# Performance work log

Hardware: AMD Instinct MI355X
Metric: run time of the kernel (lower is better)

The kernel has to match this reference:

```python
import jax, jax.numpy as jnp
import numpy as np

H = 2048        # hidden_size
NH = 32         # num_attention_heads
HD = H // NH    # head_dim
I = 8192        # intermediate_size
L = 2           # num_hidden_layers
B, S = 1, 2048
EPS = 1e-5


def _layernorm(x, gamma):
    # keras LayerNormalization(center=False): mean-subtract, var-normalize, scale by gamma (no beta)
    mu = jnp.mean(x, axis=-1, keepdims=True)
    var = jnp.mean(jnp.square(x - mu), axis=-1, keepdims=True)
    return (x - mu) * jax.lax.rsqrt(var + EPS) * gamma


def _gelu_tanh(x):
    return 0.5 * x * (1.0 + jnp.tanh(0.7978845608028654 * x * (1.0 + 0.044715 * x * x)))


def setup_inputs() -> dict:
    key = jax.random.key(0)
    ks = jax.random.split(key, 12)
    sd = 0.02
    inputs_embeds = jax.random.normal(ks[0], (B, S, H), dtype=jnp.float32)
    attention_mask = jnp.tril(jnp.ones((S, S), dtype=bool))[None, None]  # causal [1,1,S,S]
    return {
        "inputs_embeds": inputs_embeds,
        "attention_mask": attention_mask,
        "Wq": jax.random.normal(ks[1], (L, H, H), jnp.float32) * sd,
        "Wk": jax.random.normal(ks[2], (L, H, H), jnp.float32) * sd,
        "Wv": jax.random.normal(ks[3], (L, H, H), jnp.float32) * sd,
        "Wo": jax.random.normal(ks[4], (L, H, H), jnp.float32) * sd,
        "bo": jnp.zeros((L, H), jnp.float32),
        "W1": jax.random.normal(ks[5], (L, H, I), jnp.float32) * sd,
        "W2": jax.random.normal(ks[6], (L, I, H), jnp.float32) * sd,
        "b2": jnp.zeros((L, H), jnp.float32),
        "g1": jnp.ones((L, H), jnp.float32),
        "g2": jnp.ones((L, H), jnp.float32),
        "gf": jnp.ones((H,), jnp.float32),
    }


def _forward(inputs_embeds, attention_mask, Wq, Wk, Wv, Wo, bo, W1, W2, b2, g1, g2, gf):
    x = inputs_embeds
    scale = 1.0 / jnp.sqrt(jnp.float32(HD))
    for l in range(L):
        # --- attention block ---
        h = _layernorm(x, g1[l])
        q = h @ Wq[l]
        k = h @ Wk[l]
        v = h @ Wv[l]
        # split heads: [B,S,H] -> [B,NH,S,HD]
        q = q.reshape(B, S, NH, HD).transpose(0, 2, 1, 3)
        k = k.reshape(B, S, NH, HD).transpose(0, 2, 1, 3)
        v = v.reshape(B, S, NH, HD).transpose(0, 2, 1, 3)
        scores = jnp.einsum("bhqd,bhkd->bhqk", q, k) * scale
        scores = jnp.where(attention_mask, scores, jnp.float32(-1e9))
        probs = jax.nn.softmax(scores, axis=-1)
        ctx = jnp.einsum("bhqk,bhkd->bhqd", probs, v)
        ctx = ctx.transpose(0, 2, 1, 3).reshape(B, S, H)
        x = x + (ctx @ Wo[l] + bo[l])
        # --- MLP block ---
        h = _layernorm(x, g2[l])
        h = _gelu_tanh(h @ W1[l]) @ W2[l] + b2[l]
        x = x + h
    return _layernorm(x, gf)


def reference(inputs_embeds, attention_mask, Wq, Wk, Wv, Wo, bo, W1, W2, b2, g1, g2, gf):
    return _forward(inputs_embeds, attention_mask, Wq, Wk, Wv, Wo, bo, W1, W2, b2, g1, g2, gf)
```

## Files before the change

### kernel.cpp

```cpp
#include <hip/hip_runtime.h>
#include <hip/hip_bf16.h>
#include <stdint.h>


#define H_   2048
#define NH_  32
#define HD_  64
#define I_   8192
#define L_   2
#define S_   2048
#define EPS_ 1e-5f

typedef _Float16 f16;
typedef __attribute__((ext_vector_type(8))) _Float16 f16x8;
typedef __attribute__((ext_vector_type(4))) float   f32x4;

#define BF16_PROBE 0x3F803F80u

static __device__ __forceinline__ float bf2f(unsigned short b) {
  return __uint_as_float(((unsigned int)b) << 16);
}

static __device__ __forceinline__ float gelu_f(float x) {
  float y = 0.7978845608028654f * x * (1.0f + 0.044715f * x * x);
  return x / (1.0f + __expf(-2.0f * y));
}

#define GLDS(gp, lp)                                                          \
  __builtin_amdgcn_global_load_lds(                                           \
      (const __attribute__((address_space(1))) unsigned int*)(gp),            \
      (__attribute__((address_space(3))) unsigned int*)(lp), 16, 0, 0)

__global__ __launch_bounds__(256) void embed2f_k(const void* __restrict__ e,
                                                 float* __restrict__ xf,
                                                 const unsigned int* __restrict__ probe) {
  bool isbf = (*probe == BF16_PROBE);
  int i = (blockIdx.x * 256 + threadIdx.x) * 4;
  float4 o;
  if (isbf) {
    uint2 d = *(const uint2*)((const unsigned short*)e + i);
    o.x = bf2f((unsigned short)(d.x & 0xffff));
    o.y = bf2f((unsigned short)(d.x >> 16));
    o.z = bf2f((unsigned short)(d.y & 0xffff));
    o.w = bf2f((unsigned short)(d.y >> 16));
  } else {
    o = *(const float4*)((const float*)e + i);
  }
  *(float4*)(xf + i) = o;
}

template <int OUT_FINAL>
__global__ __launch_bounds__(256) void ln_k(const float* __restrict__ x,
                                            const void* __restrict__ gammav,
                                            size_t geoff,
                                            void* __restrict__ outv,
                                            const unsigned int* __restrict__ probe) {
  bool isbf = (*probe == BF16_PROBE);
  int row = blockIdx.x, t = threadIdx.x;
  const float* xr = x + (size_t)row * H_;
  float4 a = ((const float4*)xr)[t];
  float4 b = ((const float4*)xr)[t + 256];
  float s  = a.x + a.y + a.z + a.w + b.x + b.y + b.z + b.w;
  float ss = a.x*a.x + a.y*a.y + a.z*a.z + a.w*a.w
           + b.x*b.x + b.y*b.y + b.z*b.z + b.w*b.w;
#pragma unroll
  for (int m = 32; m >= 1; m >>= 1) { s += __shfl_xor(s, m); ss += __shfl_xor(ss, m); }
  __shared__ float red[8];
  if ((t & 63) == 0) { red[t >> 6] = s; red[4 + (t >> 6)] = ss; }
  __syncthreads();
  s  = red[0] + red[1] + red[2] + red[3];
  ss = red[4] + red[5] + red[6] + red[7];
  float mu   = s * (1.0f / H_);
  float rstd = rsqrtf(ss * (1.0f / H_) - mu * mu + EPS_);
  float va[8] = {a.x, a.y, a.z, a.w, b.x, b.y, b.z, b.w};
#pragma unroll
  for (int hh = 0; hh < 2; ++hh) {
    int cbase = (hh == 0) ? t * 4 : (t + 256) * 4;
#pragma unroll
    for (int j = 0; j < 4; ++j) {
      int c = cbase + j;
      float g = isbf ? bf2f(((const unsigned short*)gammav)[geoff + c])
                     : ((const float*)gammav)[geoff + c];
      float o = (va[hh * 4 + j] - mu) * rstd * g;
      size_t idx = (size_t)row * H_ + c;
      if (OUT_FINAL) {
        if (isbf) ((__hip_bfloat16*)outv)[idx] = __float2bfloat16(o);
        else      ((float*)outv)[idx] = o;
      } else {
        ((f16*)outv)[idx] = (f16)o;
      }
    }
  }
}

__global__ __launch_bounds__(256) void transp_k(const void* __restrict__ in,
                                                size_t eoff,
                                                f16* __restrict__ out, int R, int C,
                                                const unsigned int* __restrict__ probe) {
  bool isbf = (*probe == BF16_PROBE);
  __shared__ __attribute__((aligned(16))) f16 tile[64][72];
  int t = threadIdx.x;
  int r0 = blockIdx.y * 64, c0 = blockIdx.x * 64;
#pragma unroll
  for (int it = 0; it < 2; ++it) {
    int idx = it * 256 + t;
    int r = idx >> 3, c8 = (idx & 7) * 8;
    size_t goff = eoff + (size_t)(r0 + r) * C + c0 + c8;
    if (isbf) {
      uint4 d = *(const uint4*)((const unsigned short*)in + goff);
      unsigned int dw[4] = {d.x, d.y, d.z, d.w};
#pragma unroll
      for (int p = 0; p < 4; ++p) {
        tile[r][c8 + 2 * p]     = (f16)bf2f((unsigned short)(dw[p] & 0xffff));
        tile[r][c8 + 2 * p + 1] = (f16)bf2f((unsigned short)(dw[p] >> 16));
      }
    } else {
      float4 fa = *(const float4*)((const float*)in + goff);
      float4 fb = *(const float4*)((const float*)in + goff + 4);
      tile[r][c8 + 0] = (f16)fa.x; tile[r][c8 + 1] = (f16)fa.y;
      tile[r][c8 + 2] = (f16)fa.z; tile[r][c8 + 3] = (f16)fa.w;
      tile[r][c8 + 4] = (f16)fb.x; tile[r][c8 + 5] = (f16)fb.y;
      tile[r][c8 + 6] = (f16)fb.z; tile[r][c8 + 7] = (f16)fb.w;
    }
  }
  __syncthreads();
#pragma unroll
  for (int it = 0; it < 2; ++it) {
    int idx = it * 256 + t;
    int rn = idx >> 3, k8 = (idx & 7) * 8;
    f16x8 o;
#pragma unroll
    for (int j = 0; j < 8; ++j) o[j] = tile[k8 + j][rn];
    *(f16x8*)(out + (size_t)(c0 + rn) * R + r0 + k8) = o;
  }
}

template <int MODE>
__global__ __launch_bounds__(256) void gemm_k(const f16* __restrict__ A,
                                              const f16* __restrict__ Bt,
                                              f16* __restrict__ Cf,
                                              float* __restrict__ xres,
                                              const void* __restrict__ biasv,
                                              size_t beoff,
                                              int N, int K,
                                              const unsigned int* __restrict__ probe) {
  __shared__ __attribute__((aligned(16))) f16 As[128 * 32];
  __shared__ __attribute__((aligned(16))) f16 Bs[128 * 32];
  int t = threadIdx.x;
  int lane = t & 63, w = t >> 6;
  int col = lane & 15, quad = lane >> 4;
  int tm = blockIdx.x * 128, tn = blockIdx.y * 128;
  int wm = (w & 1) * 64, wn = (w >> 1) * 64;

  f32x4 acc[4][4];
#pragma unroll
  for (int i = 0; i < 4; ++i)
#pragma unroll
    for (int j = 0; j < 4; ++j) acc[i][j] = (f32x4){0.f, 0.f, 0.f, 0.f};

  const f16* Ab = A  + (size_t)(tm + (t >> 2)) * K + (t & 3) * 8;
  const f16* Bb = Bt + (size_t)(tn + (t >> 2)) * K + (t & 3) * 8;
  f16* Al = As + t * 8;
  f16* Bl = Bs + t * 8;

  for (int k0 = 0; k0 < K; k0 += 32) {
    GLDS(Ab + k0, Al);
    GLDS(Ab + (size_t)64 * K + k0, Al + 2048);
    GLDS(Bb + k0, Bl);
    GLDS(Bb + (size_t)64 * K + k0, Bl + 2048);
    __syncthreads();
    f16x8 af[4], bf[4];
#pragma unroll
    for (int i = 0; i < 4; ++i)
      af[i] = *(const f16x8*)(As + (wm + i * 16 + col) * 32 + quad * 8);
#pragma unroll
    for (int j = 0; j < 4; ++j)
      bf[j] = *(const f16x8*)(Bs + (wn + j * 16 + col) * 32 + quad * 8);
#pragma unroll
    for (int i = 0; i < 4; ++i)
#pragma unroll
      for (int j = 0; j < 4; ++j)
        acc[i][j] = __builtin_amdgcn_mfma_f32_16x16x32_f16(af[i], bf[j], acc[i][j], 0, 0, 0);
    __syncthreads();
  }

  bool isbf = false;
  if (MODE == 2) isbf = (*probe == BF16_PROBE);
#pragma unroll
  for (int i = 0; i < 4; ++i) {
    int row = tm + wm + i * 16 + quad * 4;
#pragma unroll
    for (int j = 0; j < 4; ++j) {
      int cg = tn + wn + j * 16 + col;
#pragma unroll
      for (int r = 0; r < 4; ++r) {
        float v = acc[i][j][r];
        if (MODE == 1) v = gelu_f(v);
        if (MODE <= 1) {
          Cf[(size_t)(row + r) * N + cg] = (f16)v;
        } else {
          float bb = isbf ? bf2f(((const unsigned short*)biasv)[beoff + cg])
                          : ((const float*)biasv)[beoff + cg];
          size_t idx = (size_t)(row + r) * N + cg;
          xres[idx] += v + bb;
        }
      }
    }
  }
}


#define MIDBAR()                                                              \
  asm volatile("" ::: "memory");                                              \
  __builtin_amdgcn_s_barrier();                                               \
  asm volatile("s_waitcnt lgkmcnt(0)" ::: "memory");                          \
  __builtin_amdgcn_sched_barrier(0);                                          \
  __builtin_amdgcn_s_setprio(1)

#define ENDBAR()                                                              \
  asm volatile("" ::: "memory");                                              \
  __builtin_amdgcn_s_barrier();                                               \
  __builtin_amdgcn_sched_barrier(0)

#define LDA8(AF, BUF, MH)                                                     \
  _Pragma("unroll") for (int m2 = 0; m2 < 4; ++m2)                            \
  _Pragma("unroll") for (int kk = 0; kk < 2; ++kk)                            \
    AF[m2][kk] = *(const f16x8*)(lds + (BUF) * 32768 +                        \
        (wr * 128 + (MH) * 64 + m2 * 16 + col) * 64 +                         \
        ((((kk << 2) + quad) ^ xq) << 3));

#define LDB4(BF, BUF, NH)                                                     \
  _Pragma("unroll") for (int n2 = 0; n2 < 2; ++n2)                            \
  _Pragma("unroll") for (int kk = 0; kk < 2; ++kk)                            \
    BF[n2][kk] = *(const f16x8*)(lds + 16384 + (BUF) * 32768 +                \
        (wc * 64 + (NH) * 32 + n2 * 16 + col) * 64 +                         \
        ((((kk << 2) + quad) ^ xq) << 3));

#define QMM(AF, BF, MH, NH)                                                   \
  _Pragma("unroll") for (int m2 = 0; m2 < 4; ++m2)                            \
  _Pragma("unroll") for (int n2 = 0; n2 < 2; ++n2)                            \
  _Pragma("unroll") for (int kk = 0; kk < 2; ++kk)                            \
    acc[(MH) * 4 + m2][(NH) * 2 + n2] =                                       \
        __builtin_amdgcn_mfma_f32_16x16x32_f16(                               \
            AF[m2][kk], BF[n2][kk], acc[(MH) * 4 + m2][(NH) * 2 + n2], 0, 0, 0);

template <int MODE>
__global__ __launch_bounds__(512, 2) void gemm256_k(const f16* __restrict__ A,
                                                    const f16* __restrict__ Bt,
                                                    f16* __restrict__ Cf,
                                                    int N, int K) {
  __shared__ __attribute__((aligned(16))) f16 lds[65536];
  const int t = threadIdx.x;
  const int lane = t & 63, wid = t >> 6;
  const int col = lane & 15, quad = lane >> 4;
  const int xq = lane & 7;
  const int wr = wid >> 2, wc = wid & 3;
  const int tm = blockIdx.x * 256, tn = blockIdx.y * 256;
  const int NK = K >> 6;

  f32x4 acc[8][4];
#pragma unroll
  for (int i = 0; i < 8; ++i)
#pragma unroll
    for (int j = 0; j < 4; ++j) acc[i][j] = (f32x4){0.f, 0.f, 0.f, 0.f};

  const int srow = t >> 3;
  const int gs   = (t & 7) ^ (srow & 7);
  const f16* gA = A  + (size_t)(tm + srow) * K + gs * 8;
  const f16* gB = Bt + (size_t)(tn + srow) * K + gs * 8;
  f16* lbase = lds + t * 8;

  auto STAGE = [&](int mat, int h, int u) {
    if (u >= NK) return;
    const f16* gp0 = (mat ? gB : gA) + (size_t)(h * 128) * K + u * 64;
    f16* lp = lbase + (u & 1) * 32768 + mat * 16384 + h * 8192;
    GLDS(gp0, lp);
    GLDS(gp0 + (size_t)64 * K, lp + 4096);
  };

  STAGE(1, 0, 0); STAGE(1, 1, 0); STAGE(0, 0, 0); STAGE(0, 1, 0);
  STAGE(1, 0, 1); STAGE(1, 1, 1);
  asm volatile("s_waitcnt vmcnt(4)" ::: "memory");
  __builtin_amdgcn_s_barrier();
  __builtin_amdgcn_sched_barrier(0);

  f16x8 afr[4][2], b0f[2][2], b1f[2][2];

  for (int u = 0; u < NK; ++u) {
    const int b = u & 1;
    LDA8(afr, b, 0);
    LDB4(b0f, b, 0);
    STAGE(0, 0, u + 1);
    MIDBAR();
    QMM(afr, b0f, 0, 0);
    __builtin_amdgcn_s_setprio(0);
    ENDBAR();
    LDB4(b1f, b, 1);
    STAGE(0, 1, u + 1);
    MIDBAR();
    QMM(afr, b1f, 0, 1);
    __builtin_amdgcn_s_setprio(0);
    ENDBAR();
    LDA8(afr, b, 1);
    STAGE(1, 0, u + 2);
    MIDBAR();
    QMM(afr, b1f, 1, 1);
    __builtin_amdgcn_s_setprio(0);
    ENDBAR();
    STAGE(1, 1, u + 2);
    MIDBAR();
    QMM(afr, b0f, 1, 0);
    __builtin_amdgcn_s_setprio(0);
    if (u + 2 < NK) { asm volatile("s_waitcnt vmcnt(4)" ::: "memory"); }
    else            { asm volatile("s_waitcnt vmcnt(0)" ::: "memory"); }
    ENDBAR();
  }

#pragma unroll
  for (int m = 0; m < 8; ++m) {
    int row = tm + wr * 128 + m * 16 + quad * 4;
#pragma unroll
    for (int n = 0; n < 4; ++n) {
      int cg = tn + wc * 64 + n * 16 + col;
#pragma unroll
      for (int r = 0; r < 4; ++r) {
        float v = acc[m][n][r];
        if (MODE == 1) v = gelu_f(v);
        Cf[(size_t)(row + r) * N + cg] = (f16)v;
      }
    }
  }
}

__global__ __launch_bounds__(256) void attn_k(const f16* __restrict__ qkv,
                                              f16* __restrict__ ctx) {
  __shared__ __attribute__((aligned(16))) f16 Ks[64 * 72];
  __shared__ __attribute__((aligned(16))) f16 Vt[64 * 72];
  __shared__ __attribute__((aligned(16))) f16 Ps[4 * 16 * 72];
  const int RS = 3 * H_;
  int t = threadIdx.x, w = t >> 6, lane = t & 63;
  int col = lane & 15, quad = lane >> 4;
  int head = blockIdx.y;
  int qt = (gridDim.x - 1) - blockIdx.x;
  int q0 = qt * 64;

  int qrow = q0 + w * 16 + col;
  const f16* qp = qkv + (size_t)qrow * RS + head * HD_ + quad * 8;
  f16x8 qf0 = *(const f16x8*)qp;
  f16x8 qf1 = *(const f16x8*)(qp + 32);

  f32x4 O[4];
#pragma unroll
  for (int ht = 0; ht < 4; ++ht) O[ht] = (f32x4){0.f, 0.f, 0.f, 0.f};
  f32x4 mrow = (f32x4){-1e30f, -1e30f, -1e30f, -1e30f};
  f32x4 lrow = (f32x4){0.f, 0.f, 0.f, 0.f};
  f16* pw = Ps + w * 16 * 72;

  for (int c = 0; c <= qt; ++c) {
    int k0 = c * 64;
#pragma unroll
    for (int it = 0; it < 2; ++it) {
      int idx = it * 256 + t;
      int r = idx >> 3, c8 = (idx & 7) * 8;
      const f16* kp = qkv + (size_t)(k0 + r) * RS + H_ + head * HD_ + c8;
      *(f16x8*)(Ks + r * 72 + c8) = *(const f16x8*)kp;
      const f16* vp = qkv + (size_t)(k0 + r) * RS + 2 * H_ + head * HD_ + c8;
      f16x8 vv = *(const f16x8*)vp;
#pragma unroll
      for (int j = 0; j < 8; ++j) Vt[(c8 + j) * 72 + r] = vv[j];
    }
    __syncthreads();

    f32x4 s[4];
#pragma unroll
    for (int nt = 0; nt < 4; ++nt) {
      const f16* kb = Ks + (nt * 16 + col) * 72 + quad * 8;
      f16x8 b0 = *(const f16x8*)kb;
      f16x8 b1 = *(const f16x8*)(kb + 32);
      f32x4 z = (f32x4){0.f, 0.f, 0.f, 0.f};
      z = __builtin_amdgcn_mfma_f32_16x16x32_f16(qf0, b0, z, 0, 0, 0);
      z = __builtin_amdgcn_mfma_f32_16x16x32_f16(qf1, b1, z, 0, 0, 0);
      s[nt] = z;
    }
    int rq = q0 + w * 16 + quad * 4;
#pragma unroll
    for (int nt = 0; nt < 4; ++nt)
#pragma unroll
      for (int r = 0; r < 4; ++r) {
        float sv = s[nt][r] * 0.125f;
        if (k0 + nt * 16 + col > rq + r) sv = -1e30f;
        s[nt][r] = sv;
      }
    f32x4 mx;
#pragma unroll
    for (int r = 0; r < 4; ++r)
      mx[r] = fmaxf(fmaxf(s[0][r], s[1][r]), fmaxf(s[2][r], s[3][r]));
#pragma unroll
    for (int m = 1; m <= 8; m <<= 1)
#pragma unroll
      for (int r = 0; r < 4; ++r) mx[r] = fmaxf(mx[r], __shfl_xor(mx[r], m));
    f32x4 mnew, alpha, rs;
#pragma unroll
    for (int r = 0; r < 4; ++r) {
      mnew[r]  = fmaxf(mrow[r], mx[r]);
      alpha[r] = __expf(mrow[r] - mnew[r]);
      rs[r] = 0.f;
    }
#pragma unroll
    for (int nt = 0; nt < 4; ++nt)
#pragma unroll
      for (int r = 0; r < 4; ++r) {
        float p = __expf(s[nt][r] - mnew[r]);
        s[nt][r] = p;
        rs[r] += p;
      }
#pragma unroll
    for (int m = 1; m <= 8; m <<= 1)
#pragma unroll
      for (int r = 0; r < 4; ++r) rs[r] += __shfl_xor(rs[r], m);
#pragma unroll
    for (int r = 0; r < 4; ++r) {
      lrow[r] = lrow[r] * alpha[r] + rs[r];
      mrow[r] = mnew[r];
    }
#pragma unroll
    for (int ht = 0; ht < 4; ++ht)
#pragma unroll
      for (int r = 0; r < 4; ++r) O[ht][r] *= alpha[r];

#pragma unroll
    for (int nt = 0; nt < 4; ++nt)
#pragma unroll
      for (int r = 0; r < 4; ++r)
        pw[(quad * 4 + r) * 72 + nt * 16 + col] = (f16)s[nt][r];
    const f16* pr = pw + col * 72 + quad * 8;
    f16x8 p0 = *(const f16x8*)pr;
    f16x8 p1 = *(const f16x8*)(pr + 32);
#pragma unroll
    for (int ht = 0; ht < 4; ++ht) {
      const f16* vb = Vt + (ht * 16 + col) * 72 + quad * 8;
      f16x8 v0 = *(const f16x8*)vb;
      f16x8 v1 = *(const f16x8*)(vb + 32);
      O[ht] = __builtin_amdgcn_mfma_f32_16x16x32_f16(p0, v0, O[ht], 0, 0, 0);
      O[ht] = __builtin_amdgcn_mfma_f32_16x16x32_f16(p1, v1, O[ht], 0, 0, 0);
    }
    __syncthreads();
  }

#pragma unroll
  for (int ht = 0; ht < 4; ++ht)
#pragma unroll
    for (int r = 0; r < 4; ++r) {
      int row = q0 + w * 16 + quad * 4 + r;
      int cg = head * HD_ + ht * 16 + col;
      ctx[(size_t)row * H_ + cg] = (f16)(O[ht][r] / lrow[r]);
    }
}

extern "C" void kernel_launch(void* const* d_in, const int* in_sizes, int n_in,
                              void* d_out, int out_size, void* d_ws, size_t ws_size,
                              hipStream_t stream) {
  const void* embeds = d_in[0];
  const void* Wq = d_in[2];
  const void* Wk = d_in[3];
  const void* Wv = d_in[4];
  const void* Wo = d_in[5];
  const void* bo = d_in[6];
  const void* W1 = d_in[7];
  const void* W2 = d_in[8];
  const void* b2 = d_in[9];
  const void* g1 = d_in[10];
  const void* g2 = d_in[11];
  const void* gf = d_in[12];
  const unsigned int* probe = (const unsigned int*)g1;

  char* W = (char*)d_ws;
  float* xf  = (float*)(W);
  f16* hbuf  = (f16*)(W + (16ull << 20));
  f16* qkvb  = (f16*)(W + (24ull << 20));
  f16* ctxb  = (f16*)(W + (48ull << 20));
  f16* m1b   = (f16*)(W + (24ull << 20));
  f16* Wt    = (f16*)(W + (56ull << 20));
  (void)in_sizes; (void)n_in; (void)out_size; (void)ws_size;

  embed2f_k<<<S_ * H_ / 1024, 256, 0, stream>>>(embeds, xf, probe);

  for (int l = 0; l < L_; ++l) {
    size_t wo = (size_t)l * H_ * H_;
    ln_k<0><<<S_, 256, 0, stream>>>(xf, g1, (size_t)l * H_, hbuf, probe);
    transp_k<<<dim3(H_ / 64, H_ / 64), 256, 0, stream>>>(Wq, wo, Wt, H_, H_, probe);
    transp_k<<<dim3(H_ / 64, H_ / 64), 256, 0, stream>>>(Wk, wo, Wt + (size_t)H_ * H_, H_, H_, probe);
    transp_k<<<dim3(H_ / 64, H_ / 64), 256, 0, stream>>>(Wv, wo, Wt + 2ull * H_ * H_, H_, H_, probe);
    gemm256_k<0><<<dim3(S_ / 256, 3 * H_ / 256), 512, 0, stream>>>(hbuf, Wt, qkvb, 3 * H_, H_);
    attn_k<<<dim3(S_ / 64, NH_), 256, 0, stream>>>(qkvb, ctxb);
    transp_k<<<dim3(H_ / 64, H_ / 64), 256, 0, stream>>>(Wo, wo, Wt, H_, H_, probe);
    gemm_k<2><<<dim3(S_ / 128, H_ / 128), 256, 0, stream>>>(ctxb, Wt, nullptr, xf, bo, (size_t)l * H_, H_, H_, probe);
    ln_k<0><<<S_, 256, 0, stream>>>(xf, g2, (size_t)l * H_, hbuf, probe);
    transp_k<<<dim3(I_ / 64, H_ / 64), 256, 0, stream>>>(W1, (size_t)l * H_ * I_, Wt, H_, I_, probe);
    gemm256_k<1><<<dim3(S_ / 256, I_ / 256), 512, 0, stream>>>(hbuf, Wt, m1b, I_, H_);
    transp_k<<<dim3(H_ / 64, I_ / 64), 256, 0, stream>>>(W2, (size_t)l * I_ * H_, Wt, I_, H_, probe);
    gemm_k<2><<<dim3(S_ / 128, H_ / 128), 256, 0, stream>>>(m1b, Wt, nullptr, xf, b2, (size_t)l * H_, H_, I_, probe);
  }
  ln_k<1><<<S_, 256, 0, stream>>>(xf, gf, 0, d_out, probe);
}
```

Measured before the change: 1.545 ms.

## Use split-K 256-tile GEMM with atomic residual add for output projections

Replaces the simple 128x128 GEMM used for the Wo and W2 projections with the pipelined 256x256 kernel, split four ways along K using gridDim.z. Each split atomically adds its partial product into the fp32 residual, and only split 0 adds the bias. Without the split, the N=2048 outputs would give only 64 tiles of 256x256, too few blocks for the GPU; the split raises that to 256. The cost is fp32 atomic traffic, and the order of the partial sums is no longer deterministic.

```diff
diff --git a/kernel.cpp b/kernel.cpp
--- a/kernel.cpp
+++ b/kernel.cpp
@@ -135,80 +135,6 @@
   }
 }
 
-template <int MODE>
-__global__ __launch_bounds__(256) void gemm_k(const f16* __restrict__ A,
-                                              const f16* __restrict__ Bt,
-                                              f16* __restrict__ Cf,
-                                              float* __restrict__ xres,
-                                              const void* __restrict__ biasv,
-                                              size_t beoff,
-                                              int N, int K,
-                                              const unsigned int* __restrict__ probe) {
-  __shared__ __attribute__((aligned(16))) f16 As[128 * 32];
-  __shared__ __attribute__((aligned(16))) f16 Bs[128 * 32];
-  int t = threadIdx.x;
-  int lane = t & 63, w = t >> 6;
-  int col = lane & 15, quad = lane >> 4;
-  int tm = blockIdx.x * 128, tn = blockIdx.y * 128;
-  int wm = (w & 1) * 64, wn = (w >> 1) * 64;
-
-  f32x4 acc[4][4];
-#pragma unroll
-  for (int i = 0; i < 4; ++i)
-#pragma unroll
-    for (int j = 0; j < 4; ++j) acc[i][j] = (f32x4){0.f, 0.f, 0.f, 0.f};
-
-  const f16* Ab = A  + (size_t)(tm + (t >> 2)) * K + (t & 3) * 8;
-  const f16* Bb = Bt + (size_t)(tn + (t >> 2)) * K + (t & 3) * 8;
-  f16* Al = As + t * 8;
-  f16* Bl = Bs + t * 8;
-
-  for (int k0 = 0; k0 < K; k0 += 32) {
-    GLDS(Ab + k0, Al);
-    GLDS(Ab + (size_t)64 * K + k0, Al + 2048);
-    GLDS(Bb + k0, Bl);
-    GLDS(Bb + (size_t)64 * K + k0, Bl + 2048);
-    __syncthreads();
-    f16x8 af[4], bf[4];
-#pragma unroll
-    for (int i = 0; i < 4; ++i)
-      af[i] = *(const f16x8*)(As + (wm + i * 16 + col) * 32 + quad * 8);
-#pragma unroll
-    for (int j = 0; j < 4; ++j)
-      bf[j] = *(const f16x8*)(Bs + (wn + j * 16 + col) * 32 + quad * 8);
-#pragma unroll
-    for (int i = 0; i < 4; ++i)
-#pragma unroll
-      for (int j = 0; j < 4; ++j)
-        acc[i][j] = __builtin_amdgcn_mfma_f32_16x16x32_f16(af[i], bf[j], acc[i][j], 0, 0, 0);
-    __syncthreads();
-  }
-
-  bool isbf = false;
-  if (MODE == 2) isbf = (*probe == BF16_PROBE);
-#pragma unroll
-  for (int i = 0; i < 4; ++i) {
-    int row = tm + wm + i * 16 + quad * 4;
-#pragma unroll
-    for (int j = 0; j < 4; ++j) {
-      int cg = tn + wn + j * 16 + col;
-#pragma unroll
-      for (int r = 0; r < 4; ++r) {
-        float v = acc[i][j][r];
-        if (MODE == 1) v = gelu_f(v);
-        if (MODE <= 1) {
-          Cf[(size_t)(row + r) * N + cg] = (f16)v;
-        } else {
-          float bb = isbf ? bf2f(((const unsigned short*)biasv)[beoff + cg])
-                          : ((const float*)biasv)[beoff + cg];
-          size_t idx = (size_t)(row + r) * N + cg;
-          xres[idx] += v + bb;
-        }
-      }
-    }
-  }
-}
-
 
 #define MIDBAR()                                                              \
   asm volatile("" ::: "memory");                                              \
@@ -248,7 +174,11 @@
 __global__ __launch_bounds__(512, 2) void gemm256_k(const f16* __restrict__ A,
                                                     const f16* __restrict__ Bt,
                                                     f16* __restrict__ Cf,
-                                                    int N, int K) {
+                                                    float* __restrict__ xres,
+                                                    const void* __restrict__ biasv,
+                                                    size_t beoff,
+                                                    int N, int K,
+                                                    const unsigned int* __restrict__ probe) {
   __shared__ __attribute__((aligned(16))) f16 lds[65536];
   const int t = threadIdx.x;
   const int lane = t & 63, wid = t >> 6;
@@ -256,7 +186,9 @@
   const int xq = lane & 7;
   const int wr = wid >> 2, wc = wid & 3;
   const int tm = blockIdx.x * 256, tn = blockIdx.y * 256;
-  const int NK = K >> 6;
+  const int KSP = K / (int)gridDim.z;
+  const int kb  = (int)blockIdx.z * KSP;
+  const int NK  = KSP >> 6;
 
   f32x4 acc[8][4];
 #pragma unroll
@@ -266,8 +198,8 @@
 
   const int srow = t >> 3;
   const int gs   = (t & 7) ^ (srow & 7);
-  const f16* gA = A  + (size_t)(tm + srow) * K + gs * 8;
-  const f16* gB = Bt + (size_t)(tn + srow) * K + gs * 8;
+  const f16* gA = A  + (size_t)(tm + srow) * K + kb + gs * 8;
+  const f16* gB = Bt + (size_t)(tn + srow) * K + kb + gs * 8;
   f16* lbase = lds + t * 8;
 
   auto STAGE = [&](int mat, int h, int u) {
@@ -316,6 +248,9 @@
     ENDBAR();
   }
 
+  bool isbf = false;
+  if (MODE == 2) isbf = (*probe == BF16_PROBE);
+  const bool addb = (MODE == 2) && (blockIdx.z == 0);
 #pragma unroll
   for (int m = 0; m < 8; ++m) {
     int row = tm + wr * 128 + m * 16 + quad * 4;
@@ -326,7 +261,16 @@
       for (int r = 0; r < 4; ++r) {
         float v = acc[m][n][r];
         if (MODE == 1) v = gelu_f(v);
-        Cf[(size_t)(row + r) * N + cg] = (f16)v;
+        size_t idx = (size_t)(row + r) * N + cg;
+        if (MODE <= 1) {
+          Cf[idx] = (f16)v;
+        } else {
+          if (addb) {
+            v += isbf ? bf2f(((const unsigned short*)biasv)[beoff + cg])
+                      : ((const float*)biasv)[beoff + cg];
+          }
+          atomicAdd(xres + idx, v);
+        }
       }
     }
   }
@@ -491,15 +435,15 @@
     transp_k<<<dim3(H_ / 64, H_ / 64), 256, 0, stream>>>(Wq, wo, Wt, H_, H_, probe);
     transp_k<<<dim3(H_ / 64, H_ / 64), 256, 0, stream>>>(Wk, wo, Wt + (size_t)H_ * H_, H_, H_, probe);
     transp_k<<<dim3(H_ / 64, H_ / 64), 256, 0, stream>>>(Wv, wo, Wt + 2ull * H_ * H_, H_, H_, probe);
-    gemm256_k<0><<<dim3(S_ / 256, 3 * H_ / 256), 512, 0, stream>>>(hbuf, Wt, qkvb, 3 * H_, H_);
+    gemm256_k<0><<<dim3(S_ / 256, 3 * H_ / 256), 512, 0, stream>>>(hbuf, Wt, qkvb, nullptr, nullptr, 0, 3 * H_, H_, probe);
     attn_k<<<dim3(S_ / 64, NH_), 256, 0, stream>>>(qkvb, ctxb);
     transp_k<<<dim3(H_ / 64, H_ / 64), 256, 0, stream>>>(Wo, wo, Wt, H_, H_, probe);
-    gemm_k<2><<<dim3(S_ / 128, H_ / 128), 256, 0, stream>>>(ctxb, Wt, nullptr, xf, bo, (size_t)l * H_, H_, H_, probe);
+    gemm256_k<2><<<dim3(S_ / 256, H_ / 256, 4), 512, 0, stream>>>(ctxb, Wt, nullptr, xf, bo, (size_t)l * H_, H_, H_, probe);
     ln_k<0><<<S_, 256, 0, stream>>>(xf, g2, (size_t)l * H_, hbuf, probe);
     transp_k<<<dim3(I_ / 64, H_ / 64), 256, 0, stream>>>(W1, (size_t)l * H_ * I_, Wt, H_, I_, probe);
-    gemm256_k<1><<<dim3(S_ / 256, I_ / 256), 512, 0, stream>>>(hbuf, Wt, m1b, I_, H_);
+    gemm256_k<1><<<dim3(S_ / 256, I_ / 256), 512, 0, stream>>>(hbuf, Wt, m1b, nullptr, nullptr, 0, I_, H_, probe);
     transp_k<<<dim3(H_ / 64, I_ / 64), 256, 0, stream>>>(W2, (size_t)l * I_ * H_, Wt, I_, H_, probe);
-    gemm_k<2><<<dim3(S_ / 128, H_ / 128), 256, 0, stream>>>(m1b, Wt, nullptr, xf, b2, (size_t)l * H_, H_, I_, probe);
+    gemm256_k<2><<<dim3(S_ / 256, H_ / 256, 4), 512, 0, stream>>>(m1b, Wt, nullptr, xf, b2, (size_t)l * H_, H_, I_, probe);
   }
   ln_k<1><<<S_, 256, 0, stream>>>(xf, gf, 0, d_out, probe);
 }
```

New measurement: 1.522 ms. About the same (-1.5%).
